# Kernel tuning notes

Measured on AMD Instinct MI355X. Metric: run time of the kernel, lower is better.

Reference implementation:

```python
import jax, jax.numpy as jnp
import numpy as np

N, C, T, V = 32, 128, 128, 25
HS, HT, CI = 3, 2, 32
BN_INV = float(1.0 / np.sqrt(1.0 + 1e-5))  # eval-mode BN: running_mean=0, running_var=1


def conv1x1(x, w, b):
    # x: (N,C,T,V), w: (O,C), b: (O,)
    return jnp.einsum('nctv,oc->notv', x, w) + b[None, :, None, None]


def bn(x, g, b):
    return x * (g * BN_INV)[None, :, None, None] + b[None, :, None, None]


def lrelu(x):
    return jax.nn.leaky_relu(x, 0.1)


def setup_inputs() -> dict:
    key = jax.random.key(0)
    ks = jax.random.split(key, 16)
    w = lambda k, shp: jax.random.normal(k, shp, dtype=jnp.float32) * 0.05
    inp = {
        'x': jax.random.normal(ks[0], (N, C, T, V), dtype=jnp.float32),
        # spatial attention QK projection (conv 1x1): 2*HS*CI out channels
        'w_in_s': w(ks[1], (2 * HS * CI, C)), 'b_in_s': jnp.zeros((2 * HS * CI,), jnp.float32),
        'attention0s': jnp.ones((1, HS, V, V), jnp.float32) / V,
        'alphas': jnp.ones((1, HS, 1, 1), jnp.float32),
        'w_out_s': w(ks[2], (C, HS * C)), 'b_out_s': jnp.zeros((C,), jnp.float32),
        'g_out_s': jnp.ones((C,), jnp.float32), 'be_out_s': jnp.zeros((C,), jnp.float32),
        'w_ff_s': w(ks[3], (C, C)), 'b_ff_s': jnp.zeros((C,), jnp.float32),
        'g_ff_s': jnp.ones((C,), jnp.float32), 'be_ff_s': jnp.zeros((C,), jnp.float32),
        # temporal attention QK projection: 4*HT*CI out channels
        'w_in_t': w(ks[4], (4 * HT * CI, C)), 'b_in_t': jnp.zeros((4 * HT * CI,), jnp.float32),
        'alphat_f': jnp.ones((1, HT, 1, 1), jnp.float32),
        'alphat_b': jnp.ones((1, HT, 1, 1), jnp.float32),
        'w_out_t': w(ks[5], (C, 2 * HT * C)), 'b_out_t': jnp.zeros((C,), jnp.float32),
        'g_out_t': jnp.ones((C,), jnp.float32), 'be_out_t': jnp.zeros((C,), jnp.float32),
        'w_ff_t': w(ks[6], (C, C)), 'b_ff_t': jnp.zeros((C,), jnp.float32),
        'g_ff_t': jnp.ones((C,), jnp.float32), 'be_ff_t': jnp.zeros((C,), jnp.float32),
        # TCN: 7x1 temporal conv
        'w_tcn': w(ks[7], (C, C, 7, 1)), 'b_tcn': jnp.zeros((C,), jnp.float32),
        'g_tcn': jnp.ones((C,), jnp.float32), 'be_tcn': jnp.zeros((C,), jnp.float32),
    }
    return inp


def reference(x, w_in_s, b_in_s, attention0s, alphas, w_out_s, b_out_s, g_out_s, be_out_s,
              w_ff_s, b_ff_s, g_ff_s, be_ff_s, w_in_t, b_in_t, alphat_f, alphat_b,
              w_out_t, b_out_t, g_out_t, be_out_t, w_ff_t, b_ff_t, g_ff_t, be_ff_t,
              w_tcn, b_tcn, g_tcn, be_tcn):
    n = x.shape[0]
    # ---------------- spatial attention (S_atten='free', glo_reg_s) ----------------
    att_bias = attention0s[:, :, None]            # (1,HS,1,V,V) broadcast over T
    alphas_u = alphas[:, :, None]                 # (1,HS,1,1,1)
    qk = conv1x1(x, w_in_s, b_in_s).reshape(n, 2 * HS, CI, T, V)
    q, k = qk[:, :HS], qk[:, HS:]
    att = att_bias + jnp.tanh(jnp.einsum('nsctu,nsctv->nstuv', q, k) / CI) * alphas_u  # (N,HS,T,V,V)
    y = jnp.einsum('nctu,nstuv->nsctv', x, att).reshape(n, HS * C, T, V)
    y = bn(conv1x1(y, w_out_s, b_out_s), g_out_s, be_out_s)
    y = lrelu(x + y)                               # downs1 = identity (in==out, stride 1)
    y = bn(conv1x1(y, w_ff_s, b_ff_s), g_ff_s, be_ff_s)
    s_out = lrelu(x + y)                           # downs2 = identity
    # ---------------- temporal attention (directed, T_atten='context') ----------------
    z_in = s_out                                   # parallel=False -> temporal eats s_out
    qk_t = conv1x1(z_in, w_in_t, b_in_t).reshape(n, 4 * HT, CI, T, V)
    qt, kt = qk_t[:, :2 * HT], qk_t[:, 2 * HT:]
    qt = qt.mean(-1)                               # context attention: mean over joints -> (N,2HT,CI,T)
    kt = kt.mean(-1)
    att_t = jnp.tanh(jnp.einsum('nsct,nscu->nstu', qt, kt) / CI)  # (N,2HT,T,T)
    backward_mask = jnp.triu(jnp.ones((T, T), jnp.float32))
    forward_mask = backward_mask.T
    att_f = att_t[:, :HT] * alphat_f * forward_mask
    att_b = att_t[:, HT:] * alphat_b * backward_mask
    att_t = jnp.concatenate([att_f, att_b], axis=1)               # (N,2HT,T,T)
    z = jnp.einsum('nctv,nstu->nscuv', z_in, att_t).reshape(n, 2 * HT * C, T, V)
    z = bn(conv1x1(z, w_out_t, b_out_t), g_out_t, be_out_t)
    z = lrelu(z_in + z)                            # downt1 = identity
    z = bn(conv1x1(z, w_ff_t, b_ff_t), g_ff_t, be_ff_t)
    t_out = lrelu(z_in + z)                        # downt2 = identity
    # ---------------- TCN branch ----------------
    z2 = jax.lax.conv_general_dilated(t_out, w_tcn, (1, 1), ((3, 3), (0, 0)),
                                      dimension_numbers=('NCHW', 'OIHW', 'NCHW'))
    z2 = bn(z2 + b_tcn[None, :, None, None] * 0 + b_tcn[None, :, None, None], g_tcn, be_tcn) if False else bn(z2 + b_tcn[None, :, None, None], g_tcn, be_tcn)
    out = lrelu(t_out + z2)                        # downtTCN = identity
    return out
```

## Files before the change

kernel.cpp:

```cpp
#include <hip/hip_runtime.h>
#include <cstddef>

#define Nn 32
#define Cc 128
#define Tt 128
#define Vv 25
#define BN_INV 0.9999950000374997f


typedef __attribute__((ext_vector_type(8))) short bf16x8;
typedef __attribute__((ext_vector_type(4))) float f32x4;

__device__ __forceinline__ unsigned short f2bf(float f) {
    union { float f; unsigned u; } x; x.f = f;
    return (unsigned short)((x.u + 0x7FFFu + ((x.u >> 16) & 1u)) >> 16);
}
__device__ __forceinline__ float bf2f(unsigned short s) {
    union { unsigned u; float f; } x; x.u = ((unsigned)s) << 16;
    return x.f;
}

template<int BMODE, int DMODE, int OM>
__global__ __launch_bounds__(256, 2) void gemm_k(
    const unsigned short* __restrict__ A, const void* __restrict__ Bv,
    float* __restrict__ D, unsigned short* __restrict__ Dbf,
    const float* __restrict__ resp, const float* __restrict__ bias,
    const float* __restrict__ gg, const float* __restrict__ bb,
    int M, int K, int lda, int ldb, int ldd,
    long an_stride, long bn_stride, long dn_stride, int gn, int gxn)
{
    __shared__ short Al[8*64*8];
    __shared__ short Bl[8*64*8];

    const int nwg = gridDim.x;
    const int b   = blockIdx.x;
    const int w   = (b & 7)*(nwg >> 3) + (b >> 3);
    const int n   = w / gxn;
    const int rem = w - n*gxn;
    const int mt  = rem / gn;
    const int nt  = rem - mt*gn;
    const int m0 = mt*128;
    const int j0 = nt*128;

    const unsigned short* An = A + (size_t)n*an_stride;

    const int tid = threadIdx.x;
    const int wav = tid >> 6, lane = tid & 63;
    const int lq = lane >> 4, l16 = lane & 15;

    const int sm  = tid >> 1, skh = tid & 1;
    const int scol = tid & 127, skq = tid >> 7;
    const int bcol = j0 + scol;

    int bo = 0, bv_ = 0;
    if (BMODE == 3) { bo = bcol/25; bv_ = bcol - 25*bo; }

    f32x4 acc[2][8];
    #pragma unroll
    for (int i = 0; i < 2; ++i)
        #pragma unroll
        for (int c = 0; c < 8; ++c) acc[i][c] = (f32x4){0.f,0.f,0.f,0.f};

    for (int k0 = 0; k0 < K; k0 += 32) {
        bf16x8 a0 = (bf16x8){0,0,0,0,0,0,0,0}, a1 = a0;
        {
            int mg = m0 + sm;
            if (mg < M) {
                const unsigned short* ap = An + (size_t)mg*lda + k0 + skh*16;
                a0 = *(const bf16x8*)ap;
                a1 = *(const bf16x8*)(ap + 8);
            }
        }
        unsigned short bq[16];
        if (BMODE == 0) {
            const unsigned short* Bn = (const unsigned short*)Bv + (size_t)n*bn_stride;
            #pragma unroll
            for (int j = 0; j < 16; ++j)
                bq[j] = Bn[(size_t)(k0 + skq*16 + j)*ldb + bcol];
        } else if (BMODE == 4) {
            const float* Bf = (const float*)Bv + (size_t)n*bn_stride;
            #pragma unroll
            for (int j = 0; j < 16; ++j)
                bq[j] = f2bf(Bf[(size_t)(k0 + skq*16 + j)*ldb + bcol]);
        } else if (BMODE == 1) {
            const unsigned short* Bn = (const unsigned short*)Bv + (size_t)n*bn_stride;
            int kb = k0 + skq*16;
            int kidx = kb >> 7, c0 = kb & 127;
            int e = bcol + (kidx - 3)*25;
            bool ok = ((unsigned)e < 3200u);
            #pragma unroll
            for (int j = 0; j < 16; ++j)
                bq[j] = ok ? Bn[(size_t)(c0 + j)*3200 + e] : (unsigned short)0;
        } else {
            const unsigned short* Bn = (const unsigned short*)Bv + (size_t)n*bn_stride;
            int kb = k0 + skq*16;
            int h = kb >> 7, t0 = kb & 127;
            const unsigned short* bp = Bn + (size_t)h*409600 + (size_t)bo*3200
                                          + (size_t)t0*25 + bv_;
            #pragma unroll
            for (int j = 0; j < 16; ++j) bq[j] = bp[j*25];
        }

        __syncthreads();
        {
            short* Ap = Al + ((size_t)((sm>>4)*64 + (sm&15) + 32*skh))*8;
            *(bf16x8*)Ap = a0;
            *(bf16x8*)(Ap + 128) = a1;
        }
        {
            short* Bp = Bl + ((size_t)((scol>>4)*64 + (scol&15) + 32*skq))*8;
            bf16x8 p0, p1;
            #pragma unroll
            for (int j = 0; j < 8; ++j) { p0[j] = (short)bq[j]; p1[j] = (short)bq[8+j]; }
            *(bf16x8*)Bp = p0;
            *(bf16x8*)(Bp + 128) = p1;
        }
        __syncthreads();

        bf16x8 afr[2], bfr[8];
        afr[0] = *(const bf16x8*)(Al + ((size_t)((2*wav+0)*64 + lane))*8);
        afr[1] = *(const bf16x8*)(Al + ((size_t)((2*wav+1)*64 + lane))*8);
        #pragma unroll
        for (int c = 0; c < 8; ++c)
            bfr[c] = *(const bf16x8*)(Bl + ((size_t)(c*64 + lane))*8);
        #pragma unroll
        for (int i = 0; i < 2; ++i)
            #pragma unroll
            for (int c = 0; c < 8; ++c)
                acc[i][c] = __builtin_amdgcn_mfma_f32_16x16x32_bf16(
                    afr[i], bfr[c], acc[i][c], 0, 0, 0);
    }

    #pragma unroll
    for (int i = 0; i < 2; ++i) {
        const int mbase = m0 + (2*wav + i)*16 + lq*4;
        #pragma unroll
        for (int ct = 0; ct < 8; ++ct) {
            const int col = j0 + ct*16 + l16;
            if (DMODE == 0) {
                #pragma unroll
                for (int r = 0; r < 4; ++r) {
                    const int mg = mbase + r;
                    if (mg < M) {
                        const size_t addr = (size_t)mg*ldd + col + (size_t)n*dn_stride;
                        float val = acc[i][ct][r] + (bias ? bias[mg] : 0.f);
                        if (gg) {
                            val = val*(gg[mg]*BN_INV) + bb[mg] + resp[addr];
                            val = val > 0.f ? val : 0.1f*val;
                        }
                        if (OM != 1) D[addr] = val;
                        if (OM >= 1) Dbf[addr] = f2bf(val);
                    }
                }
            } else {
                const int c = col/25, v = col - 25*c;
                const float bi = bias ? bias[c] : 0.f;
                float gv = 0.f, b2 = 0.f;
                if (gg) { gv = gg[c]*BN_INV; b2 = bb[c]; }
                #pragma unroll
                for (int r = 0; r < 4; ++r) {
                    const int u = mbase + r;
                    const size_t addr = (size_t)c*3200 + (size_t)u*25 + v
                                      + (size_t)n*dn_stride;
                    float val = acc[i][ct][r] + bi;
                    if (gg) {
                        val = val*gv + b2 + resp[addr];
                        val = val > 0.f ? val : 0.1f*val;
                    }
                    if (OM != 1) D[addr] = val;
                    if (OM >= 1) Dbf[addr] = f2bf(val);
                }
            }
        }
    }
}

__global__ void k_prep(const float* __restrict__ wis, const float* __restrict__ wos,
                       const float* __restrict__ wfs, const float* __restrict__ wit,
                       const float* __restrict__ wot, const float* __restrict__ wft,
                       const float* __restrict__ wtc, unsigned short* __restrict__ W) {
    int i = blockIdx.x*256 + threadIdx.x;
    if (i < 24576) { W[i] = f2bf(wis[i]); return; }          i -= 24576;
    if (i < 49152) { W[24576 + i] = f2bf(wos[i]); return; }  i -= 49152;
    if (i < 16384) { W[73728 + i] = f2bf(wfs[i]); return; }  i -= 16384;
    if (i < 32768) { W[90112 + i] = f2bf(wit[i]); return; }  i -= 32768;
    if (i < 65536) {
        int ho = i >> 7, c = i & 127; int h = ho >> 7, o = ho & 127;
        W[122880 + i] = f2bf(wot[o*512 + h*128 + c]); return; } i -= 65536;
    if (i < 16384) { W[188416 + i] = f2bf(wft[i]); return; } i -= 16384;
    if (i < 114688) {
        int o = i / 896; int r = i - o*896; int kidx = r >> 7, c = r & 127;
        W[204800 + i] = f2bf(wtc[(o*128 + c)*7 + kidx]); }
}

__global__ void k_att_s(const unsigned short* __restrict__ qk,
                        const float* __restrict__ att0,
                        const float* __restrict__ alphas,
                        unsigned short* __restrict__ att) {
    int b = blockIdx.x;
    int n = b / (3*Tt); int rem = b - n*(3*Tt); int s = rem / Tt; int t = rem - s*Tt;
    __shared__ float qs[32*Vv], ks[32*Vv];
    const unsigned short* qp = qk + (size_t)n*614400 + (size_t)(s*32)*3200 + t*25;
    const unsigned short* kp = qk + (size_t)n*614400 + (size_t)(96 + s*32)*3200 + t*25;
    for (int i = threadIdx.x; i < 32*Vv; i += 256) {
        int c = i / Vv, v = i - c*Vv;
        qs[i] = bf2f(qp[(size_t)c*3200 + v]);
        ks[i] = bf2f(kp[(size_t)c*3200 + v]);
    }
    __syncthreads();
    float alpha = alphas[s];
    for (int i = threadIdx.x; i < Vv*Vv; i += 256) {
        int u = i / Vv, v = i - u*Vv;
        float a = 0.f;
        #pragma unroll
        for (int c = 0; c < 32; ++c) a += qs[c*Vv + u] * ks[c*Vv + v];
        att[(size_t)n*240000 + (size_t)s*80000 + (size_t)t*625 + i] =
            f2bf(att0[s*625 + i] + tanhf(a * (1.f/32.f)) * alpha);
    }
}

__global__ __launch_bounds__(256, 2) void k_eins_mfma(
    const float* __restrict__ X, const unsigned short* __restrict__ att,
    unsigned short* __restrict__ y2)
{
    __shared__ short Xf[128*128];
    __shared__ short Bf[7*4*64*8];

    const int n  = blockIdx.x >> 5;
    const int t0 = (blockIdx.x & 31) * 4;
    const int tid = threadIdx.x;
    const int wav = tid >> 6, lane = tid & 63;
    const int lq = lane >> 4, l16 = lane & 15;

    for (int i = tid; i < 7*4*64; i += 256)
        *(bf16x8*)(Bf + (size_t)i*8) = (bf16x8){0,0,0,0,0,0,0,0};

    const float* xp = X + (size_t)n*409600;
    for (int i = tid; i < 8192; i += 256) {
        int u2 = (i & 15)*2, tl = (i >> 4) & 3, c = i >> 6;
        float f0 = 0.f, f1 = 0.f;
        if (u2 < 25) {
            const float* p = xp + (size_t)c*3200 + (t0 + tl)*25 + u2;
            f0 = p[0];
            if (u2 < 24) f1 = p[1];
        }
        unsigned pk = (unsigned)f2bf(f0) | ((unsigned)f2bf(f1) << 16);
        int byte = (i*4) ^ ((c & 7) << 4);
        *(unsigned*)((char*)Xf + byte) = pk;
    }
    __syncthreads();

    bf16x8 afr[2][4];
    #pragma unroll
    for (int i = 0; i < 2; ++i) {
        const int c = (2*wav + i)*16 + l16;
        #pragma unroll
        for (int ks = 0; ks < 4; ++ks) {
            int byte = ((c*128 + ks*32 + lq*8)*2) ^ ((c & 7) << 4);
            afr[i][ks] = *(const bf16x8*)((const char*)Xf + byte);
        }
    }

    for (int s = 0; s < 3; ++s) {
        const unsigned short* ap = att + (size_t)n*240000 + (size_t)s*80000
                                       + (size_t)t0*625;
        for (int j = tid; j < 2500; j += 256) {
            int tl = j / 625, r = j - tl*625;
            int u = r / 25, v = r - u*25;
            int col = tl*25 + v;
            int l = ((u >> 3) << 4) | (col & 15);
            int nt = col >> 4;
            Bf[(size_t)((nt*4 + tl)*64 + l)*8 + (u & 7)] = (short)ap[j];
        }
        __syncthreads();

        f32x4 acc[2][7];
        #pragma unroll
        for (int i = 0; i < 2; ++i)
            #pragma unroll
            for (int nt = 0; nt < 7; ++nt) acc[i][nt] = (f32x4){0.f,0.f,0.f,0.f};

        #pragma unroll
        for (int ks = 0; ks < 4; ++ks) {
            bf16x8 bfr[7];
            #pragma unroll
            for (int nt = 0; nt < 7; ++nt)
                bfr[nt] = *(const bf16x8*)(Bf + (size_t)((nt*4 + ks)*64 + lane)*8);
            #pragma unroll
            for (int i = 0; i < 2; ++i)
                #pragma unroll
                for (int nt = 0; nt < 7; ++nt)
                    acc[i][nt] = __builtin_amdgcn_mfma_f32_16x16x32_bf16(
                        afr[i][ks], bfr[nt], acc[i][nt], 0, 0, 0);
        }

        unsigned short* yb = y2 + (size_t)n*1228800 + (size_t)(s*128)*3200 + t0*25;
        #pragma unroll
        for (int i = 0; i < 2; ++i) {
            const int row = (2*wav + i)*16 + lq*4;
            #pragma unroll
            for (int nt = 0; nt < 7; ++nt) {
                const int col = nt*16 + l16;
                if (col < 100) {
                    unsigned short* yp = yb + (size_t)row*3200 + col;
                    #pragma unroll
                    for (int r = 0; r < 4; ++r)
                        yp[(size_t)r*3200] = f2bf(acc[i][nt][r]);
                }
            }
        }
        __syncthreads();
    }
}

__global__ void k_mean(const float* __restrict__ X, unsigned short* __restrict__ xb) {
    int idx = blockIdx.x*256 + threadIdx.x;
    if (idx >= Nn*Cc*Tt) return;
    const float* p = X + (size_t)idx*25;
    float s = 0.f;
    #pragma unroll
    for (int v = 0; v < Vv; ++v) s += p[v];
    xb[idx] = f2bf(s * (1.f/25.f));
}

__global__ void k_att_t(const float* __restrict__ qkt, const float* __restrict__ af,
                        const float* __restrict__ ab, unsigned short* __restrict__ attb) {
    int n = blockIdx.x >> 2, h = blockIdx.x & 3;
    __shared__ float qs[32*Tt], ks[32*Tt];
    const float* qp = qkt + (size_t)n*32768 + (size_t)(h*32)*128;
    const float* kp = qkt + (size_t)n*32768 + (size_t)(128 + h*32)*128;
    for (int i = threadIdx.x; i < 32*Tt; i += 256) { qs[i] = qp[i]; ks[i] = kp[i]; }
    __syncthreads();
    float alpha = (h < 2) ? af[h] : ab[h-2];
    for (int i = threadIdx.x; i < Tt*Tt; i += 256) {
        int u = i >> 7, t = i & 127;
        bool keep = (h < 2) ? (t >= u) : (t <= u);
        float val = 0.f;
        if (keep) {
            float a = 0.f;
            #pragma unroll
            for (int c = 0; c < 32; ++c) a += qs[c*Tt + t] * ks[c*Tt + u];
            val = tanhf(a * (1.f/32.f)) * alpha;
        }
        attb[(size_t)n*65536 + (size_t)u*512 + h*128 + t] = f2bf(val);
    }
}

extern "C" void kernel_launch(void* const* d_in, const int* in_sizes, int n_in,
                              void* d_out, int out_size, void* d_ws, size_t ws_size,
                              hipStream_t stream) {
    const float* x       = (const float*)d_in[0];
    const float* w_in_s  = (const float*)d_in[1];
    const float* b_in_s  = (const float*)d_in[2];
    const float* att0s   = (const float*)d_in[3];
    const float* alphas  = (const float*)d_in[4];
    const float* w_out_s = (const float*)d_in[5];
    const float* b_out_s = (const float*)d_in[6];
    const float* g_out_s = (const float*)d_in[7];
    const float* be_out_s= (const float*)d_in[8];
    const float* w_ff_s  = (const float*)d_in[9];
    const float* b_ff_s  = (const float*)d_in[10];
    const float* g_ff_s  = (const float*)d_in[11];
    const float* be_ff_s = (const float*)d_in[12];
    const float* w_in_t  = (const float*)d_in[13];
    const float* b_in_t  = (const float*)d_in[14];
    const float* alphat_f= (const float*)d_in[15];
    const float* alphat_b= (const float*)d_in[16];
    const float* w_out_t = (const float*)d_in[17];
    const float* b_out_t = (const float*)d_in[18];
    const float* g_out_t = (const float*)d_in[19];
    const float* be_out_t= (const float*)d_in[20];
    const float* w_ff_t  = (const float*)d_in[21];
    const float* b_ff_t  = (const float*)d_in[22];
    const float* g_ff_t  = (const float*)d_in[23];
    const float* be_ff_t = (const float*)d_in[24];
    const float* w_tcn   = (const float*)d_in[25];
    const float* b_tcn   = (const float*)d_in[26];
    const float* g_tcn   = (const float*)d_in[27];
    const float* be_tcn  = (const float*)d_in[28];

    float* ws = (float*)d_ws;
    unsigned short* WB    = (unsigned short*)ws;
    unsigned short* QKBF  = (unsigned short*)(ws + 200000);
    unsigned short* S1BF  = (unsigned short*)(ws + 200000);
    unsigned short* ATSB  = (unsigned short*)(ws + 10030400);
    unsigned short* Y2BF  = (unsigned short*)(ws + 13870400);
    float*          SOUT  = ws + 33531200;
    unsigned short* ATTB  = (unsigned short*)(ws + 200000);
    unsigned short* XBARB = (unsigned short*)(ws + 1300000);
    float*          QKT   = ws + 1600000;
    unsigned short* TMPB  = (unsigned short*)(ws + 2700000);
    unsigned short* T1BF  = (unsigned short*)(ws + 46638400);
    float*          TOUT  = ws + 2700000;
    unsigned short* TOUTB = (unsigned short*)(ws + 15810000);
    float* out = (float*)d_out;

    unsigned short* wbis = WB;
    unsigned short* wbos = WB + 24576;
    unsigned short* wbfs = WB + 73728;
    unsigned short* wbit = WB + 90112;
    unsigned short* wbot = WB + 122880;
    unsigned short* wbft = WB + 188416;
    unsigned short* wbtc = WB + 204800;

    dim3 blk(256);
    const float* NUL = nullptr;

    k_prep<<<1248, blk, 0, stream>>>(w_in_s, w_out_s, w_ff_s, w_in_t,
                                     w_out_t, w_ff_t, w_tcn, WB);

    gemm_k<4,0,1><<<1600, blk, 0, stream>>>(
        wbis, x, nullptr, QKBF, NUL, b_in_s, NUL, NUL,
        192, 128, 128, 3200, 3200, 0L, 409600L, 614400L, 25, 50);
    k_att_s<<<Nn*3*Tt, blk, 0, stream>>>(QKBF, att0s, alphas, ATSB);
    k_eins_mfma<<<dim3(Nn*32), blk, 0, stream>>>(x, ATSB, Y2BF);
    gemm_k<0,0,1><<<800, blk, 0, stream>>>(
        wbos, Y2BF, nullptr, S1BF, x, b_out_s, g_out_s, be_out_s,
        128, 384, 384, 3200, 3200, 0L, 1228800L, 409600L, 25, 25);
    gemm_k<0,0,0><<<800, blk, 0, stream>>>(
        wbfs, S1BF, SOUT, nullptr, x, b_ff_s, g_ff_s, be_ff_s,
        128, 128, 128, 3200, 3200, 0L, 409600L, 409600L, 25, 25);

    k_mean<<<2048, blk, 0, stream>>>(SOUT, XBARB);
    gemm_k<0,0,0><<<64, blk, 0, stream>>>(
        wbit, XBARB, QKT, nullptr, NUL, b_in_t, NUL, NUL,
        256, 128, 128, 128, 128, 0L, 16384L, 32768L, 1, 2);
    k_att_t<<<Nn*4, blk, 0, stream>>>(QKT, alphat_f, alphat_b, ATTB);
    gemm_k<4,0,1><<<3200, blk, 0, stream>>>(
        wbot, SOUT, nullptr, TMPB, NUL, NUL, NUL, NUL,
        512, 128, 128, 3200, 3200, 0L, 409600L, 1638400L, 25, 100);
    gemm_k<3,2,1><<<800, blk, 0, stream>>>(
        ATTB, TMPB, nullptr, T1BF, SOUT, b_out_t, g_out_t, be_out_t,
        128, 512, 512, 3200, 3200, 65536L, 1638400L, 409600L, 25, 25);
    gemm_k<0,0,2><<<800, blk, 0, stream>>>(
        wbft, T1BF, TOUT, TOUTB, SOUT, b_ff_t, g_ff_t, be_ff_t,
        128, 128, 128, 3200, 3200, 0L, 409600L, 409600L, 25, 25);

    gemm_k<1,0,0><<<800, blk, 0, stream>>>(
        wbtc, TOUTB, out, nullptr, TOUT, b_tcn, g_tcn, be_tcn,
        128, 896, 896, 3200, 3200, 0L, 409600L, 409600L, 25, 25);
}
```

Before: 710.0 us.

## Transpose B operands to K-contiguous layout and load tiles via global_load_lds

Intermediate bf16 activations are now written K-major (column-contiguous along the reduction dimension) by producer kernels. This lets the GEMM load B tiles, and A tiles, with 16-byte direct global-to-LDS loads instead of strided scalar gathers. The TCN input gets zero-padded halos from a new k_zpad kernel, which removes the per-element bounds checks. Launch bounds are raised to 4 waves per SIMD. The cost is scattered transposed stores in the epilogues and an extra small kernel launch.

```diff
diff --git a/kernel.cpp b/kernel.cpp
--- a/kernel.cpp
+++ b/kernel.cpp
@@ -9,6 +9,7 @@
 
 
 typedef __attribute__((ext_vector_type(8))) short bf16x8;
+typedef __attribute__((ext_vector_type(4))) short short4v;
 typedef __attribute__((ext_vector_type(4))) float f32x4;
 
 __device__ __forceinline__ unsigned short f2bf(float f) {
@@ -20,17 +21,24 @@
     return x.f;
 }
 
+__device__ __forceinline__ void gload16(const unsigned short* g, short* l) {
+    __builtin_amdgcn_global_load_lds(
+        (const __attribute__((address_space(1))) void*)g,
+        (__attribute__((address_space(3))) void*)l, 16, 0, 0);
+}
+
 template<int BMODE, int DMODE, int OM>
-__global__ __launch_bounds__(256, 2) void gemm_k(
+__global__ __launch_bounds__(256, 4) void gemm_k(
     const unsigned short* __restrict__ A, const void* __restrict__ Bv,
     float* __restrict__ D, unsigned short* __restrict__ Dbf,
     const float* __restrict__ resp, const float* __restrict__ bias,
     const float* __restrict__ gg, const float* __restrict__ bb,
     int M, int K, int lda, int ldb, int ldd,
-    long an_stride, long bn_stride, long dn_stride, int gn, int gxn)
+    long an_stride, long bn_stride, long dn_stride, long dbfn,
+    int gn, int gxn)
 {
-    __shared__ short Al[8*64*8];
-    __shared__ short Bl[8*64*8];
+    __shared__ __attribute__((aligned(16))) short Al[8*64*8];
+    __shared__ __attribute__((aligned(16))) short Bl[8*64*8];
 
     const int nwg = gridDim.x;
     const int b   = blockIdx.x;
@@ -48,12 +56,28 @@
     const int wav = tid >> 6, lane = tid & 63;
     const int lq = lane >> 4, l16 = lane & 15;
 
-    const int sm  = tid >> 1, skh = tid & 1;
+    const int la = lane & 15;
+    const int ka = (lane >> 4) << 3;
+    const unsigned short* gA0 = An + (size_t)(m0 + (2*wav+0)*16 + la)*lda + ka;
+    const unsigned short* gA1 = An + (size_t)(m0 + (2*wav+1)*16 + la)*lda + ka;
+    short* lA0 = Al + (size_t)((2*wav+0)*64)*8;
+    short* lA1 = Al + (size_t)((2*wav+1)*64)*8;
+    short* lB0 = Bl + (size_t)((2*wav+0)*64)*8;
+    short* lB1 = Bl + (size_t)((2*wav+1)*64)*8;
+    const unsigned short* BnU = (const unsigned short*)Bv + (size_t)n*bn_stride;
+    const int cb0 = j0 + (2*wav+0)*16 + la;
+    const int cb1 = j0 + (2*wav+1)*16 + la;
+    const unsigned short* gB0 = nullptr;
+    const unsigned short* gB1 = nullptr;
+    if (BMODE == 0) {
+        gB0 = BnU + (size_t)cb0*ldb + ka;
+        gB1 = BnU + (size_t)cb1*ldb + ka;
+    } else if (BMODE == 1 || BMODE == 3) {
+        gB0 = BnU + (size_t)cb0*128 + ka;
+        gB1 = BnU + (size_t)cb1*128 + ka;
+    }
     const int scol = tid & 127, skq = tid >> 7;
     const int bcol = j0 + scol;
-
-    int bo = 0, bv_ = 0;
-    if (BMODE == 3) { bo = bcol/25; bv_ = bcol - 25*bo; }
 
     f32x4 acc[2][8];
     #pragma unroll
@@ -62,58 +86,35 @@
         for (int c = 0; c < 8; ++c) acc[i][c] = (f32x4){0.f,0.f,0.f,0.f};
 
     for (int k0 = 0; k0 < K; k0 += 32) {
-        bf16x8 a0 = (bf16x8){0,0,0,0,0,0,0,0}, a1 = a0;
-        {
-            int mg = m0 + sm;
-            if (mg < M) {
-                const unsigned short* ap = An + (size_t)mg*lda + k0 + skh*16;
-                a0 = *(const bf16x8*)ap;
-                a1 = *(const bf16x8*)(ap + 8);
-            }
-        }
-        unsigned short bq[16];
+        bf16x8 b0r, b1r;
+        if (BMODE == 4) {
+            const float* Bf = (const float*)Bv + (size_t)n*bn_stride;
+            #pragma unroll
+            for (int j = 0; j < 8; ++j)
+                b0r[j] = (short)f2bf(Bf[(size_t)(k0 + skq*16 + j)*ldb + bcol]);
+            #pragma unroll
+            for (int j = 0; j < 8; ++j)
+                b1r[j] = (short)f2bf(Bf[(size_t)(k0 + skq*16 + 8 + j)*ldb + bcol]);
+        }
+
+        __syncthreads();
+        gload16(gA0 + k0, lA0);
+        gload16(gA1 + k0, lA1);
         if (BMODE == 0) {
-            const unsigned short* Bn = (const unsigned short*)Bv + (size_t)n*bn_stride;
-            #pragma unroll
-            for (int j = 0; j < 16; ++j)
-                bq[j] = Bn[(size_t)(k0 + skq*16 + j)*ldb + bcol];
-        } else if (BMODE == 4) {
-            const float* Bf = (const float*)Bv + (size_t)n*bn_stride;
-            #pragma unroll
-            for (int j = 0; j < 16; ++j)
-                bq[j] = f2bf(Bf[(size_t)(k0 + skq*16 + j)*ldb + bcol]);
+            gload16(gB0 + k0, lB0);
+            gload16(gB1 + k0, lB1);
         } else if (BMODE == 1) {
-            const unsigned short* Bn = (const unsigned short*)Bv + (size_t)n*bn_stride;
-            int kb = k0 + skq*16;
-            int kidx = kb >> 7, c0 = kb & 127;
-            int e = bcol + (kidx - 3)*25;
-            bool ok = ((unsigned)e < 3200u);
-            #pragma unroll
-            for (int j = 0; j < 16; ++j)
-                bq[j] = ok ? Bn[(size_t)(c0 + j)*3200 + e] : (unsigned short)0;
+            const int off = ((k0 >> 7) - 3)*3200 + (k0 & 127);
+            gload16(gB0 + off, lB0);
+            gload16(gB1 + off, lB1);
+        } else if (BMODE == 3) {
+            const int off = (k0 >> 7)*409600 + (k0 & 127);
+            gload16(gB0 + off, lB0);
+            gload16(gB1 + off, lB1);
         } else {
-            const unsigned short* Bn = (const unsigned short*)Bv + (size_t)n*bn_stride;
-            int kb = k0 + skq*16;
-            int h = kb >> 7, t0 = kb & 127;
-            const unsigned short* bp = Bn + (size_t)h*409600 + (size_t)bo*3200
-                                          + (size_t)t0*25 + bv_;
-            #pragma unroll
-            for (int j = 0; j < 16; ++j) bq[j] = bp[j*25];
-        }
-
-        __syncthreads();
-        {
-            short* Ap = Al + ((size_t)((sm>>4)*64 + (sm&15) + 32*skh))*8;
-            *(bf16x8*)Ap = a0;
-            *(bf16x8*)(Ap + 128) = a1;
-        }
-        {
             short* Bp = Bl + ((size_t)((scol>>4)*64 + (scol&15) + 32*skq))*8;
-            bf16x8 p0, p1;
-            #pragma unroll
-            for (int j = 0; j < 8; ++j) { p0[j] = (short)bq[j]; p1[j] = (short)bq[8+j]; }
-            *(bf16x8*)Bp = p0;
-            *(bf16x8*)(Bp + 128) = p1;
+            *(bf16x8*)Bp = b0r;
+            *(bf16x8*)(Bp + 128) = b1r;
         }
         __syncthreads();
 
@@ -152,7 +153,22 @@
                         if (OM >= 1) Dbf[addr] = f2bf(val);
                     }
                 }
-            } else {
+            } else if (DMODE == 1) {
+                short4v pk;
+                #pragma unroll
+                for (int r = 0; r < 4; ++r) {
+                    const int mg = mbase + r;
+                    const size_t addr = (size_t)mg*ldd + col + (size_t)n*dn_stride;
+                    float val = acc[i][ct][r] + (bias ? bias[mg] : 0.f);
+                    if (gg) {
+                        val = val*(gg[mg]*BN_INV) + bb[mg] + resp[addr];
+                        val = val > 0.f ? val : 0.1f*val;
+                    }
+                    if (OM != 1) D[addr] = val;
+                    pk[r] = (short)f2bf(val);
+                }
+                *(short4v*)(Dbf + (size_t)col*128 + mbase + (size_t)n*dbfn) = pk;
+            } else if (DMODE == 2) {
                 const int c = col/25, v = col - 25*c;
                 const float bi = bias ? bias[c] : 0.f;
                 float gv = 0.f, b2 = 0.f;
@@ -160,15 +176,21 @@
                 #pragma unroll
                 for (int r = 0; r < 4; ++r) {
                     const int u = mbase + r;
-                    const size_t addr = (size_t)c*3200 + (size_t)u*25 + v
-                                      + (size_t)n*dn_stride;
                     float val = acc[i][ct][r] + bi;
                     if (gg) {
-                        val = val*gv + b2 + resp[addr];
+                        val = val*gv + b2 + resp[(size_t)c*3200 + (size_t)u*25 + v
+                                                 + (size_t)n*dn_stride];
                         val = val > 0.f ? val : 0.1f*val;
                     }
-                    if (OM != 1) D[addr] = val;
-                    if (OM >= 1) Dbf[addr] = f2bf(val);
+                    Dbf[(size_t)(u*25 + v)*128 + c + (size_t)n*dbfn] = f2bf(val);
+                }
+            } else {
+                const int t = col/25, v = col - 25*t;
+                #pragma unroll
+                for (int r = 0; r < 4; ++r) {
+                    const int mg = mbase + r;
+                    float val = acc[i][ct][r] + (bias ? bias[mg] : 0.f);
+                    Dbf[((size_t)mg*25 + v)*128 + t + (size_t)n*dbfn] = f2bf(val);
                 }
             }
         }
@@ -193,6 +215,16 @@
         W[204800 + i] = f2bf(wtc[(o*128 + c)*7 + kidx]); }
 }
 
+__global__ void k_zpad(unsigned short* __restrict__ p) {
+    int i = blockIdx.x*256 + threadIdx.x;
+    if (i >= 76800) return;
+    int chunk = i*8;
+    int n = chunk / 19200;
+    int r = chunk - n*19200;
+    size_t addr = (size_t)n*428800 + (size_t)(r < 9600 ? r : 419200 + (r - 9600));
+    *(bf16x8*)(p + addr) = (bf16x8){0,0,0,0,0,0,0,0};
+}
+
 __global__ void k_att_s(const unsigned short* __restrict__ qk,
                         const float* __restrict__ att0,
                         const float* __restrict__ alphas,
@@ -294,7 +326,7 @@
                         afr[i][ks], bfr[nt], acc[i][nt], 0, 0, 0);
         }
 
-        unsigned short* yb = y2 + (size_t)n*1228800 + (size_t)(s*128)*3200 + t0*25;
+        unsigned short* yb = y2 + (size_t)n*1228800;
         #pragma unroll
         for (int i = 0; i < 2; ++i) {
             const int row = (2*wav + i)*16 + lq*4;
@@ -302,10 +334,10 @@
             for (int nt = 0; nt < 7; ++nt) {
                 const int col = nt*16 + l16;
                 if (col < 100) {
-                    unsigned short* yp = yb + (size_t)row*3200 + col;
+                    short4v pk;
                     #pragma unroll
-                    for (int r = 0; r < 4; ++r)
-                        yp[(size_t)r*3200] = f2bf(acc[i][nt][r]);
+                    for (int r = 0; r < 4; ++r) pk[r] = (short)f2bf(acc[i][nt][r]);
+                    *(short4v*)(yb + (size_t)(t0*25 + col)*384 + s*128 + row) = pk;
                 }
             }
         }
@@ -320,7 +352,8 @@
     float s = 0.f;
     #pragma unroll
     for (int v = 0; v < Vv; ++v) s += p[v];
-    xb[idx] = f2bf(s * (1.f/25.f));
+    int n = idx >> 14, rem = idx & 16383, c = rem >> 7, t = rem & 127;
+    xb[(size_t)n*16384 + (size_t)t*128 + c] = f2bf(s * (1.f/25.f));
 }
 
 __global__ void k_att_t(const float* __restrict__ qkt, const float* __restrict__ af,
@@ -385,6 +418,8 @@
     unsigned short* S1BF  = (unsigned short*)(ws + 200000);
     unsigned short* ATSB  = (unsigned short*)(ws + 10030400);
     unsigned short* Y2BF  = (unsigned short*)(ws + 13870400);
+    unsigned short* TOUTBP= (unsigned short*)(ws + 23710000);
+    unsigned short* TOUTB = TOUTBP + 9600;
     float*          SOUT  = ws + 33531200;
     unsigned short* ATTB  = (unsigned short*)(ws + 200000);
     unsigned short* XBARB = (unsigned short*)(ws + 1300000);
@@ -392,7 +427,6 @@
     unsigned short* TMPB  = (unsigned short*)(ws + 2700000);
     unsigned short* T1BF  = (unsigned short*)(ws + 46638400);
     float*          TOUT  = ws + 2700000;
-    unsigned short* TOUTB = (unsigned short*)(ws + 15810000);
     float* out = (float*)d_out;
 
     unsigned short* wbis = WB;
@@ -411,32 +445,33 @@
 
     gemm_k<4,0,1><<<1600, blk, 0, stream>>>(
         wbis, x, nullptr, QKBF, NUL, b_in_s, NUL, NUL,
-        192, 128, 128, 3200, 3200, 0L, 409600L, 614400L, 25, 50);
+        192, 128, 128, 3200, 3200, 0L, 409600L, 614400L, 614400L, 25, 50);
     k_att_s<<<Nn*3*Tt, blk, 0, stream>>>(QKBF, att0s, alphas, ATSB);
     k_eins_mfma<<<dim3(Nn*32), blk, 0, stream>>>(x, ATSB, Y2BF);
-    gemm_k<0,0,1><<<800, blk, 0, stream>>>(
+    gemm_k<0,1,1><<<800, blk, 0, stream>>>(
         wbos, Y2BF, nullptr, S1BF, x, b_out_s, g_out_s, be_out_s,
-        128, 384, 384, 3200, 3200, 0L, 1228800L, 409600L, 25, 25);
+        128, 384, 384, 384, 3200, 0L, 1228800L, 409600L, 409600L, 25, 25);
     gemm_k<0,0,0><<<800, blk, 0, stream>>>(
         wbfs, S1BF, SOUT, nullptr, x, b_ff_s, g_ff_s, be_ff_s,
-        128, 128, 128, 3200, 3200, 0L, 409600L, 409600L, 25, 25);
+        128, 128, 128, 128, 3200, 0L, 409600L, 409600L, 409600L, 25, 25);
 
     k_mean<<<2048, blk, 0, stream>>>(SOUT, XBARB);
     gemm_k<0,0,0><<<64, blk, 0, stream>>>(
         wbit, XBARB, QKT, nullptr, NUL, b_in_t, NUL, NUL,
-        256, 128, 128, 128, 128, 0L, 16384L, 32768L, 1, 2);
+        256, 128, 128, 128, 128, 0L, 16384L, 32768L, 32768L, 1, 2);
     k_att_t<<<Nn*4, blk, 0, stream>>>(QKT, alphat_f, alphat_b, ATTB);
-    gemm_k<4,0,1><<<3200, blk, 0, stream>>>(
+    gemm_k<4,3,1><<<3200, blk, 0, stream>>>(
         wbot, SOUT, nullptr, TMPB, NUL, NUL, NUL, NUL,
-        512, 128, 128, 3200, 3200, 0L, 409600L, 1638400L, 25, 100);
+        512, 128, 128, 3200, 3200, 0L, 409600L, 1638400L, 1638400L, 25, 100);
     gemm_k<3,2,1><<<800, blk, 0, stream>>>(
         ATTB, TMPB, nullptr, T1BF, SOUT, b_out_t, g_out_t, be_out_t,
-        128, 512, 512, 3200, 3200, 65536L, 1638400L, 409600L, 25, 25);
-    gemm_k<0,0,2><<<800, blk, 0, stream>>>(
+        128, 512, 512, 0, 3200, 65536L, 1638400L, 409600L, 409600L, 25, 25);
+    k_zpad<<<300, blk, 0, stream>>>(TOUTBP);
+    gemm_k<0,1,2><<<800, blk, 0, stream>>>(
         wbft, T1BF, TOUT, TOUTB, SOUT, b_ff_t, g_ff_t, be_ff_t,
-        128, 128, 128, 3200, 3200, 0L, 409600L, 409600L, 25, 25);
+        128, 128, 128, 128, 3200, 0L, 409600L, 409600L, 428800L, 25, 25);
 
     gemm_k<1,0,0><<<800, blk, 0, stream>>>(
         wbtc, TOUTB, out, nullptr, TOUT, b_tcn, g_tcn, be_tcn,
-        128, 896, 896, 3200, 3200, 0L, 409600L, 409600L, 25, 25);
-}
+        128, 896, 896, 0, 3200, 0L, 428800L, 409600L, 409600L, 25, 25);
+}
```

Measured after the change: 1.006 ms. 1.42x slower.
